# Kernel optimization log

Measured on AMD Instinct MI355X. Metric: run time of the kernel, lower is better.

The kernel has to match this reference:

```python
import jax, jax.numpy as jnp
import numpy as np

# Conv config matching init_kwargs
C_IN, C_OUT = 128, 256
KH, KW = 3, 3
STRIDE = (1, 1)
PADDING = ((1, 1), (1, 1))
DILATION = (1, 1)
B, H, W = 32, 56, 56


def setup_inputs() -> dict:
    key = jax.random.key(0)
    k1, k2, k3 = jax.random.split(key, 3)
    x = jax.random.normal(k1, (B, C_IN, H, W), dtype=jnp.float32)
    # Flattened weight as stored by Conv2DUF: conv.weight.view(O,-1).t() -> [C*kh*kw, O]
    weight = jax.random.normal(k2, (C_IN * KH * KW, C_OUT), dtype=jnp.float32) * 0.02
    bias = jax.random.normal(k3, (C_OUT,), dtype=jnp.float32) * 0.02
    return {"x": x, "weight": weight, "bias": bias}


def reference(x, weight, bias):
    # Conv2DUF computes unfold(x) @ weight + bias, which is exactly a 2D
    # cross-correlation with the original conv kernel. Recover the [O,C,kh,kw]
    # kernel from the flattened [C*kh*kw, O] matrix and use the fused conv
    # primitive (same math, no giant im2col buffer).
    kernel = weight.T.reshape(C_OUT, C_IN, KH, KW)
    out = jax.lax.conv_general_dilated(
        x, kernel,
        window_strides=STRIDE,
        padding=PADDING,
        rhs_dilation=DILATION,
        dimension_numbers=("NCHW", "OIHW", "NCHW"),
    )
    return out + bias[None, :, None, None]
```

## Files before the change

kernel.cpp:

```cpp
#include <hip/hip_runtime.h>
#include <stdint.h>


#define C_INQ 128
#define C_OUTQ 256
#define HDIM 56
#define WDIM 56
#define BDIM 32
#define HP 58
#define WP 58
#define HWPIX (HDIM * WDIM)
#define GSTRIDE (BDIM * HP * WP * 8)
#define XT_ELEMS ((size_t)16 * GSTRIDE)
#define XT_BYTES (XT_ELEMS * 2)

typedef __bf16 bf16x8 __attribute__((ext_vector_type(8)));
typedef unsigned short ushort8 __attribute__((ext_vector_type(8)));
typedef float floatx4 __attribute__((ext_vector_type(4)));

__device__ __forceinline__ unsigned short f2bf(float f) {
  union { float f; unsigned int u; } v; v.f = f;
  unsigned int u = v.u;
  unsigned int r = u + 0x7FFFu + ((u >> 16) & 1u);
  return (unsigned short)(r >> 16);
}
__device__ __forceinline__ unsigned int pack2(float a, float b) {
  return (unsigned int)f2bf(a) | ((unsigned int)f2bf(b) << 16);
}

__global__ __launch_bounds__(256) void pad_transpose_kernel(
    const float* __restrict__ x, unsigned short* __restrict__ xt) {
  const int blk = blockIdx.x;
  const int b = blk / HP;
  const int hp = blk - b * HP;
  const int t = threadIdx.x;
  uint4* __restrict__ xt4 = (uint4*)xt;
  if (hp == 0 || hp == HP - 1) {
    for (int i = t; i < 16 * WP; i += 256) {
      int g = i / WP, wp = i - g * WP;
      xt4[((size_t)(g * BDIM + b) * HP + hp) * WP + wp] = make_uint4(0, 0, 0, 0);
    }
    return;
  }
  const int h = hp - 1;
  if (t < 224) {
    const int g = t / 14;
    const int w4 = (t - g * 14) * 4;
    const float* xp = x + ((size_t)b * C_INQ + g * 8) * HWPIX + h * WDIM + w4;
    float4 L0 = *(const float4*)(xp);
    float4 L1 = *(const float4*)(xp + HWPIX);
    float4 L2 = *(const float4*)(xp + 2 * HWPIX);
    float4 L3 = *(const float4*)(xp + 3 * HWPIX);
    float4 L4 = *(const float4*)(xp + 4 * HWPIX);
    float4 L5 = *(const float4*)(xp + 5 * HWPIX);
    float4 L6 = *(const float4*)(xp + 6 * HWPIX);
    float4 L7 = *(const float4*)(xp + 7 * HWPIX);
    uint4* dst = xt4 + ((size_t)(g * BDIM + b) * HP + hp) * WP + 1 + w4;
    dst[0] = make_uint4(pack2(L0.x, L1.x), pack2(L2.x, L3.x),
                        pack2(L4.x, L5.x), pack2(L6.x, L7.x));
    dst[1] = make_uint4(pack2(L0.y, L1.y), pack2(L2.y, L3.y),
                        pack2(L4.y, L5.y), pack2(L6.y, L7.y));
    dst[2] = make_uint4(pack2(L0.z, L1.z), pack2(L2.z, L3.z),
                        pack2(L4.z, L5.z), pack2(L6.z, L7.z));
    dst[3] = make_uint4(pack2(L0.w, L1.w), pack2(L2.w, L3.w),
                        pack2(L4.w, L5.w), pack2(L6.w, L7.w));
  } else {
    const int r = t - 224;
    const int g = r >> 1;
    const int wp = (r & 1) * (WP - 1);
    xt4[((size_t)(g * BDIM + b) * HP + hp) * WP + wp] = make_uint4(0, 0, 0, 0);
  }
}

__global__ __launch_bounds__(256) void weight_transform_kernel(
    const float* __restrict__ w, unsigned short* __restrict__ wt) {
  const int bx = blockIdx.x;
  const int khw = bx >> 4;
  const int r4 = bx & 15;
  const int n0w = (r4 >> 2) * 64;
  const int c32 = (r4 & 3) * 32;
  const int t = threadIdx.x;
  __shared__ float lds[32 * 66];
#pragma unroll
  for (int r = 0; r < 8; ++r) {
    int idx = r * 256 + t;
    int n = idx & 63, c = idx >> 6;
    lds[c * 66 + n] = w[(size_t)((c32 + c) * 9 + khw) * C_OUTQ + n0w + n];
  }
  __syncthreads();
  {
    int n = t >> 2, c8 = (t & 3) * 8;
    const float* s = lds + c8 * 66 + n;
    uint4 o;
    o.x = pack2(s[0],   s[66]);
    o.y = pack2(s[132], s[198]);
    o.z = pack2(s[264], s[330]);
    o.w = pack2(s[396], s[462]);
    *(uint4*)(wt + (size_t)khw * (C_OUTQ * C_INQ) + (size_t)(n0w + n) * C_INQ + c32 + c8) = o;
  }
}

#define BM 128
#define BN 256
#define BK 32
#define STEPS 36

__global__ __launch_bounds__(256, 2) void conv_gemm_kernel(
    const unsigned short* __restrict__ xt,
    const unsigned short* __restrict__ wt,
    const float* __restrict__ bias,
    float* __restrict__ out) {
  __shared__ __align__(16) unsigned short ldsA[3 * BM * BK];
  __shared__ __align__(16) unsigned short ldsB[3 * BN * BK];

  const int t = threadIdx.x;
  const int lane = t & 63;
  const int wave = t >> 6;
  const int tile_m = blockIdx.x;

  int gbaseA[2], gbaseB[4];
#pragma unroll
  for (int r = 0; r < 2; ++r) {
    int g = r * 256 + t;
    int row = g >> 2;
    int kpart = (g & 3) ^ (row & 3);
    int pix = tile_m * BM + row;
    int b = pix / HWPIX;
    int p = pix - b * HWPIX;
    int h = p / WDIM;
    int w = p - h * WDIM;
    gbaseA[r] = kpart * GSTRIDE + ((b * HP + h) * WP + w) * 8;
  }
#pragma unroll
  for (int r = 0; r < 4; ++r) {
    int g = r * 256 + t;
    int row = g >> 2;
    int kpart = (g & 3) ^ (row & 3);
    gbaseB[r] = row * C_INQ + kpart * 8;
  }

  const int wm = (wave >> 1) * 64;
  const int wn = (wave & 1) * 128;
  const int mrow = lane & 15;
  const int quad = lane >> 4;

  int aoff[4], boff[8];
#pragma unroll
  for (int i = 0; i < 4; ++i) {
    int row = wm + i * 16 + mrow;
    aoff[i] = row * BK + ((quad ^ (row & 3)) * 8);
  }
#pragma unroll
  for (int j = 0; j < 8; ++j) {
    int row = wn + j * 16 + mrow;
    boff[j] = row * BK + ((quad ^ (row & 3)) * 8);
  }

  const int ldst = wave * 64 * 8;

  floatx4 acc[4][8] = {};

  auto stage = [&](int s2, int bufc) {
    const int khw = s2 >> 2;
    const int cq = s2 & 3;
    const int kh = khw / 3;
    const int kw = khw - kh * 3;
    const int koffA = cq * 4 * GSTRIDE + (kh * WP + kw) * 8;
    const int koffB = khw * (C_OUTQ * C_INQ) + cq * 32;
#pragma unroll
    for (int r = 0; r < 2; ++r)
      __builtin_amdgcn_global_load_lds(
          (const __attribute__((address_space(1))) unsigned int*)(xt + gbaseA[r] + koffA),
          (__attribute__((address_space(3))) unsigned int*)(ldsA + bufc * (BM * BK) + r * 2048 + ldst),
          16, 0, 0);
#pragma unroll
    for (int r = 0; r < 4; ++r)
      __builtin_amdgcn_global_load_lds(
          (const __attribute__((address_space(1))) unsigned int*)(wt + gbaseB[r] + koffB),
          (__attribute__((address_space(3))) unsigned int*)(ldsB + bufc * (BN * BK) + r * 2048 + ldst),
          16, 0, 0);
  };

  auto compute_step = [&](int bufc) {
    const unsigned short* A = ldsA + bufc * (BM * BK);
    const unsigned short* B = ldsB + bufc * (BN * BK);
    bf16x8 afr[4], bfr[8];
#pragma unroll
    for (int i = 0; i < 4; ++i)
      afr[i] = __builtin_bit_cast(bf16x8, *(const ushort8*)(A + aoff[i]));
#pragma unroll
    for (int j = 0; j < 8; ++j)
      bfr[j] = __builtin_bit_cast(bf16x8, *(const ushort8*)(B + boff[j]));
#pragma unroll
    for (int i = 0; i < 4; ++i)
#pragma unroll
      for (int j = 0; j < 8; ++j)
        acc[i][j] = __builtin_amdgcn_mfma_f32_16x16x32_bf16(afr[i], bfr[j], acc[i][j], 0, 0, 0);
  };

#define K_STEP(S, BUF, VM, DOSTAGE)                                  \
  {                                                                  \
    asm volatile("s_waitcnt vmcnt(" VM ")" ::: "memory");            \
    __builtin_amdgcn_s_barrier();                                    \
    compute_step(BUF);                                               \
    __builtin_amdgcn_s_barrier();                                    \
    if (DOSTAGE) stage((S) + 3, BUF);                                \
  }

  stage(0, 0);
  stage(1, 1);
  stage(2, 2);

#pragma unroll 1
  for (int so = 0; so < 11; ++so) {
    const int s = so * 3;
    K_STEP(s, 0, "12", true);
    K_STEP(s + 1, 1, "12", true);
    K_STEP(s + 2, 2, "12", true);
  }
  K_STEP(33, 0, "12", false);
  K_STEP(34, 1, "6", false);
  K_STEP(35, 2, "0", false);
#undef K_STEP

  float bv[8];
#pragma unroll
  for (int jn = 0; jn < 8; ++jn) bv[jn] = bias[wn + jn * 16 + mrow];
#pragma unroll
  for (int i = 0; i < 4; ++i) {
    const int mbase = tile_m * BM + wm + i * 16 + quad * 4;
    const int b = mbase / HWPIX;
    const int p = mbase - b * HWPIX;
    float* obase = out + (size_t)b * (C_OUTQ * HWPIX) + p;
#pragma unroll
    for (int jn = 0; jn < 8; ++jn) {
      const int ng = wn + jn * 16 + mrow;
      floatx4 v = acc[i][jn];
      v[0] += bv[jn]; v[1] += bv[jn]; v[2] += bv[jn]; v[3] += bv[jn];
      *(floatx4*)(obase + (size_t)ng * HWPIX) = v;
    }
  }
}

extern "C" void kernel_launch(void* const* d_in, const int* in_sizes, int n_in,
                              void* d_out, int out_size, void* d_ws, size_t ws_size,
                              hipStream_t stream) {
  const float* x    = (const float*)d_in[0];
  const float* w    = (const float*)d_in[1];
  const float* bias = (const float*)d_in[2];
  float* out = (float*)d_out;

  unsigned short* xt = (unsigned short*)d_ws;
  unsigned short* wt = (unsigned short*)((char*)d_ws + XT_BYTES);

  hipLaunchKernelGGL(pad_transpose_kernel, dim3(BDIM * HP), dim3(256), 0, stream, x, xt);
  hipLaunchKernelGGL(weight_transform_kernel, dim3(144), dim3(256), 0, stream, w, wt);
  hipLaunchKernelGGL(conv_gemm_kernel, dim3(784), dim3(256), 0, stream, xt, wt, bias, out);
}
```

Baseline: 234.4 us.

## Merge prep kernels, double-buffer LDS, new swizzle, remap tiles, raise MFMA priority

Folds the input pad/transpose and weight transform into one launch to save a kernel launch. The GEMM moves from triple to double LDS buffering, which cuts LDS use from 72KB to 48KB per block. It also changes the bank swizzle to XOR with (row>>1)&3, remaps block IDs so that consecutive blocks are spread across tiles, and wraps the MFMA loop in s_setprio. The shallower pipeline risks exposing more global-load latency.

```diff
diff --git a/kernel.cpp b/kernel.cpp
--- a/kernel.cpp
+++ b/kernel.cpp
@@ -28,115 +28,117 @@
   return (unsigned int)f2bf(a) | ((unsigned int)f2bf(b) << 16);
 }
 
-__global__ __launch_bounds__(256) void pad_transpose_kernel(
-    const float* __restrict__ x, unsigned short* __restrict__ xt) {
-  const int blk = blockIdx.x;
-  const int b = blk / HP;
-  const int hp = blk - b * HP;
+#define PAD_BLOCKS (BDIM * HP)
+__global__ __launch_bounds__(256) void prep_kernel(
+    const float* __restrict__ x, unsigned short* __restrict__ xt,
+    const float* __restrict__ w, unsigned short* __restrict__ wt) {
   const int t = threadIdx.x;
-  uint4* __restrict__ xt4 = (uint4*)xt;
-  if (hp == 0 || hp == HP - 1) {
-    for (int i = t; i < 16 * WP; i += 256) {
-      int g = i / WP, wp = i - g * WP;
+  if (blockIdx.x < PAD_BLOCKS) {
+    const int blk = blockIdx.x;
+    const int b = blk / HP;
+    const int hp = blk - b * HP;
+    uint4* __restrict__ xt4 = (uint4*)xt;
+    if (hp == 0 || hp == HP - 1) {
+      for (int i = t; i < 16 * WP; i += 256) {
+        int g = i / WP, wp = i - g * WP;
+        xt4[((size_t)(g * BDIM + b) * HP + hp) * WP + wp] = make_uint4(0, 0, 0, 0);
+      }
+      return;
+    }
+    const int h = hp - 1;
+    if (t < 224) {
+      const int g = t / 14;
+      const int w4 = (t - g * 14) * 4;
+      const float* xp = x + ((size_t)b * C_INQ + g * 8) * HWPIX + h * WDIM + w4;
+      float4 L0 = *(const float4*)(xp);
+      float4 L1 = *(const float4*)(xp + HWPIX);
+      float4 L2 = *(const float4*)(xp + 2 * HWPIX);
+      float4 L3 = *(const float4*)(xp + 3 * HWPIX);
+      float4 L4 = *(const float4*)(xp + 4 * HWPIX);
+      float4 L5 = *(const float4*)(xp + 5 * HWPIX);
+      float4 L6 = *(const float4*)(xp + 6 * HWPIX);
+      float4 L7 = *(const float4*)(xp + 7 * HWPIX);
+      uint4* dst = xt4 + ((size_t)(g * BDIM + b) * HP + hp) * WP + 1 + w4;
+      dst[0] = make_uint4(pack2(L0.x, L1.x), pack2(L2.x, L3.x),
+                          pack2(L4.x, L5.x), pack2(L6.x, L7.x));
+      dst[1] = make_uint4(pack2(L0.y, L1.y), pack2(L2.y, L3.y),
+                          pack2(L4.y, L5.y), pack2(L6.y, L7.y));
+      dst[2] = make_uint4(pack2(L0.z, L1.z), pack2(L2.z, L3.z),
+                          pack2(L4.z, L5.z), pack2(L6.z, L7.z));
+      dst[3] = make_uint4(pack2(L0.w, L1.w), pack2(L2.w, L3.w),
+                          pack2(L4.w, L5.w), pack2(L6.w, L7.w));
+    } else {
+      const int r = t - 224;
+      const int g = r >> 1;
+      const int wp = (r & 1) * (WP - 1);
       xt4[((size_t)(g * BDIM + b) * HP + hp) * WP + wp] = make_uint4(0, 0, 0, 0);
     }
-    return;
-  }
-  const int h = hp - 1;
-  if (t < 224) {
-    const int g = t / 14;
-    const int w4 = (t - g * 14) * 4;
-    const float* xp = x + ((size_t)b * C_INQ + g * 8) * HWPIX + h * WDIM + w4;
-    float4 L0 = *(const float4*)(xp);
-    float4 L1 = *(const float4*)(xp + HWPIX);
-    float4 L2 = *(const float4*)(xp + 2 * HWPIX);
-    float4 L3 = *(const float4*)(xp + 3 * HWPIX);
-    float4 L4 = *(const float4*)(xp + 4 * HWPIX);
-    float4 L5 = *(const float4*)(xp + 5 * HWPIX);
-    float4 L6 = *(const float4*)(xp + 6 * HWPIX);
-    float4 L7 = *(const float4*)(xp + 7 * HWPIX);
-    uint4* dst = xt4 + ((size_t)(g * BDIM + b) * HP + hp) * WP + 1 + w4;
-    dst[0] = make_uint4(pack2(L0.x, L1.x), pack2(L2.x, L3.x),
-                        pack2(L4.x, L5.x), pack2(L6.x, L7.x));
-    dst[1] = make_uint4(pack2(L0.y, L1.y), pack2(L2.y, L3.y),
-                        pack2(L4.y, L5.y), pack2(L6.y, L7.y));
-    dst[2] = make_uint4(pack2(L0.z, L1.z), pack2(L2.z, L3.z),
-                        pack2(L4.z, L5.z), pack2(L6.z, L7.z));
-    dst[3] = make_uint4(pack2(L0.w, L1.w), pack2(L2.w, L3.w),
-                        pack2(L4.w, L5.w), pack2(L6.w, L7.w));
   } else {
-    const int r = t - 224;
-    const int g = r >> 1;
-    const int wp = (r & 1) * (WP - 1);
-    xt4[((size_t)(g * BDIM + b) * HP + hp) * WP + wp] = make_uint4(0, 0, 0, 0);
-  }
-}
-
-__global__ __launch_bounds__(256) void weight_transform_kernel(
-    const float* __restrict__ w, unsigned short* __restrict__ wt) {
-  const int bx = blockIdx.x;
-  const int khw = bx >> 4;
-  const int r4 = bx & 15;
-  const int n0w = (r4 >> 2) * 64;
-  const int c32 = (r4 & 3) * 32;
-  const int t = threadIdx.x;
-  __shared__ float lds[32 * 66];
-#pragma unroll
-  for (int r = 0; r < 8; ++r) {
-    int idx = r * 256 + t;
-    int n = idx & 63, c = idx >> 6;
-    lds[c * 66 + n] = w[(size_t)((c32 + c) * 9 + khw) * C_OUTQ + n0w + n];
-  }
-  __syncthreads();
-  {
-    int n = t >> 2, c8 = (t & 3) * 8;
-    const float* s = lds + c8 * 66 + n;
-    uint4 o;
-    o.x = pack2(s[0],   s[66]);
-    o.y = pack2(s[132], s[198]);
-    o.z = pack2(s[264], s[330]);
-    o.w = pack2(s[396], s[462]);
-    *(uint4*)(wt + (size_t)khw * (C_OUTQ * C_INQ) + (size_t)(n0w + n) * C_INQ + c32 + c8) = o;
+    const int bx = blockIdx.x - PAD_BLOCKS;
+    const int khw = bx >> 4;
+    const int r4 = bx & 15;
+    const int n0w = (r4 >> 2) * 64;
+    const int c32 = (r4 & 3) * 32;
+    __shared__ float lds[32 * 66];
+#pragma unroll
+    for (int r = 0; r < 8; ++r) {
+      int idx = r * 256 + t;
+      int n = idx & 63, c = idx >> 6;
+      lds[c * 66 + n] = w[(size_t)((c32 + c) * 9 + khw) * C_OUTQ + n0w + n];
+    }
+    __syncthreads();
+    {
+      int n = t >> 2, c8 = (t & 3) * 8;
+      const float* s = lds + c8 * 66 + n;
+      uint4 o;
+      o.x = pack2(s[0],   s[66]);
+      o.y = pack2(s[132], s[198]);
+      o.z = pack2(s[264], s[330]);
+      o.w = pack2(s[396], s[462]);
+      *(uint4*)(wt + (size_t)khw * (C_OUTQ * C_INQ) + (size_t)(n0w + n) * C_INQ + c32 + c8) = o;
+    }
   }
 }
 
 #define BM 128
 #define BN 256
 #define BK 32
-#define STEPS 36
+#define NSTEP 36
+#define ABUF 4096
+#define BBUF 8192
 
 __global__ __launch_bounds__(256, 2) void conv_gemm_kernel(
     const unsigned short* __restrict__ xt,
     const unsigned short* __restrict__ wt,
     const float* __restrict__ bias,
     float* __restrict__ out) {
-  __shared__ __align__(16) unsigned short ldsA[3 * BM * BK];
-  __shared__ __align__(16) unsigned short ldsB[3 * BN * BK];
+  __shared__ __align__(16) unsigned short ldsA[2 * ABUF];
+  __shared__ __align__(16) unsigned short ldsB[2 * BBUF];
 
   const int t = threadIdx.x;
   const int lane = t & 63;
   const int wave = t >> 6;
-  const int tile_m = blockIdx.x;
+  const int tile_m = ((int)blockIdx.x & 7) * 98 + ((int)blockIdx.x >> 3);
 
   int gbaseA[2], gbaseB[4];
 #pragma unroll
   for (int r = 0; r < 2; ++r) {
     int g = r * 256 + t;
     int row = g >> 2;
-    int kpart = (g & 3) ^ (row & 3);
+    int kg = (g & 3) ^ ((row >> 1) & 3);
     int pix = tile_m * BM + row;
     int b = pix / HWPIX;
     int p = pix - b * HWPIX;
     int h = p / WDIM;
     int w = p - h * WDIM;
-    gbaseA[r] = kpart * GSTRIDE + ((b * HP + h) * WP + w) * 8;
+    gbaseA[r] = kg * GSTRIDE + ((b * HP + h) * WP + w) * 8;
   }
 #pragma unroll
   for (int r = 0; r < 4; ++r) {
     int g = r * 256 + t;
     int row = g >> 2;
-    int kpart = (g & 3) ^ (row & 3);
-    gbaseB[r] = row * C_INQ + kpart * 8;
+    int kg = (g & 3) ^ ((row >> 1) & 3);
+    gbaseB[r] = row * C_INQ + kg * 8;
   }
 
   const int wm = (wave >> 1) * 64;
@@ -147,81 +149,76 @@
   int aoff[4], boff[8];
 #pragma unroll
   for (int i = 0; i < 4; ++i) {
-    int row = wm + i * 16 + mrow;
-    aoff[i] = row * BK + ((quad ^ (row & 3)) * 8);
+    int r = wm + i * 16 + mrow;
+    aoff[i] = r * BK + ((quad ^ ((r >> 1) & 3)) * 8);
   }
 #pragma unroll
   for (int j = 0; j < 8; ++j) {
-    int row = wn + j * 16 + mrow;
-    boff[j] = row * BK + ((quad ^ (row & 3)) * 8);
-  }
-
-  const int ldst = wave * 64 * 8;
+    int n = wn + j * 16 + mrow;
+    boff[j] = n * BK + ((quad ^ ((n >> 1) & 3)) * 8);
+  }
 
   floatx4 acc[4][8] = {};
 
-  auto stage = [&](int s2, int bufc) {
-    const int khw = s2 >> 2;
-    const int cq = s2 & 3;
-    const int kh = khw / 3;
-    const int kw = khw - kh * 3;
+  auto stage = [&](int kt, int buf) {
+    const int khw = kt >> 2, cq = kt & 3;
+    const int kh = khw / 3, kw = khw - kh * 3;
     const int koffA = cq * 4 * GSTRIDE + (kh * WP + kw) * 8;
     const int koffB = khw * (C_OUTQ * C_INQ) + cq * 32;
 #pragma unroll
     for (int r = 0; r < 2; ++r)
       __builtin_amdgcn_global_load_lds(
           (const __attribute__((address_space(1))) unsigned int*)(xt + gbaseA[r] + koffA),
-          (__attribute__((address_space(3))) unsigned int*)(ldsA + bufc * (BM * BK) + r * 2048 + ldst),
+          (__attribute__((address_space(3))) unsigned int*)(ldsA + buf * ABUF + (r * 256 + t) * 8),
           16, 0, 0);
 #pragma unroll
     for (int r = 0; r < 4; ++r)
       __builtin_amdgcn_global_load_lds(
           (const __attribute__((address_space(1))) unsigned int*)(wt + gbaseB[r] + koffB),
-          (__attribute__((address_space(3))) unsigned int*)(ldsB + bufc * (BN * BK) + r * 2048 + ldst),
+          (__attribute__((address_space(3))) unsigned int*)(ldsB + buf * BBUF + (r * 256 + t) * 8),
           16, 0, 0);
   };
 
-  auto compute_step = [&](int bufc) {
-    const unsigned short* A = ldsA + bufc * (BM * BK);
-    const unsigned short* B = ldsB + bufc * (BN * BK);
+#define BC8(p) __builtin_bit_cast(bf16x8, *(const ushort8*)(p))
+
+  auto compute = [&](int buf) {
+    const unsigned short* A = ldsA + buf * ABUF;
+    const unsigned short* B = ldsB + buf * BBUF;
     bf16x8 afr[4], bfr[8];
 #pragma unroll
-    for (int i = 0; i < 4; ++i)
-      afr[i] = __builtin_bit_cast(bf16x8, *(const ushort8*)(A + aoff[i]));
-#pragma unroll
-    for (int j = 0; j < 8; ++j)
-      bfr[j] = __builtin_bit_cast(bf16x8, *(const ushort8*)(B + boff[j]));
+    for (int i = 0; i < 4; ++i) afr[i] = BC8(A + aoff[i]);
+#pragma unroll
+    for (int j = 0; j < 8; ++j) bfr[j] = BC8(B + boff[j]);
+    __builtin_amdgcn_s_setprio(1);
 #pragma unroll
     for (int i = 0; i < 4; ++i)
 #pragma unroll
       for (int j = 0; j < 8; ++j)
         acc[i][j] = __builtin_amdgcn_mfma_f32_16x16x32_bf16(afr[i], bfr[j], acc[i][j], 0, 0, 0);
+    __builtin_amdgcn_s_setprio(0);
   };
 
-#define K_STEP(S, BUF, VM, DOSTAGE)                                  \
+#define K_STEP(KT, BUF, VM, DOSTAGE)                                 \
   {                                                                  \
     asm volatile("s_waitcnt vmcnt(" VM ")" ::: "memory");            \
     __builtin_amdgcn_s_barrier();                                    \
-    compute_step(BUF);                                               \
+    compute(BUF);                                                    \
     __builtin_amdgcn_s_barrier();                                    \
-    if (DOSTAGE) stage((S) + 3, BUF);                                \
+    if (DOSTAGE) stage((KT) + 2, BUF);                               \
   }
 
   stage(0, 0);
   stage(1, 1);
-  stage(2, 2);
 
 #pragma unroll 1
-  for (int so = 0; so < 11; ++so) {
-    const int s = so * 3;
-    K_STEP(s, 0, "12", true);
-    K_STEP(s + 1, 1, "12", true);
-    K_STEP(s + 2, 2, "12", true);
-  }
-  K_STEP(33, 0, "12", false);
-  K_STEP(34, 1, "6", false);
-  K_STEP(35, 2, "0", false);
+  for (int so = 0; so < 17; ++so) {
+    K_STEP(so * 2, 0, "6", true);
+    K_STEP(so * 2 + 1, 1, "6", true);
+  }
+  K_STEP(34, 0, "6", false);
+  K_STEP(35, 1, "0", false);
 #undef K_STEP
+#undef BC8
 
   float bv[8];
 #pragma unroll
@@ -253,7 +250,8 @@
   unsigned short* xt = (unsigned short*)d_ws;
   unsigned short* wt = (unsigned short*)((char*)d_ws + XT_BYTES);
 
-  hipLaunchKernelGGL(pad_transpose_kernel, dim3(BDIM * HP), dim3(256), 0, stream, x, xt);
-  hipLaunchKernelGGL(weight_transform_kernel, dim3(144), dim3(256), 0, stream, w, wt);
-  hipLaunchKernelGGL(conv_gemm_kernel, dim3(784), dim3(256), 0, stream, xt, wt, bias, out);
-}
+  hipLaunchKernelGGL(prep_kernel, dim3(PAD_BLOCKS + 144), dim3(256), 0, stream,
+                     x, xt, w, wt);
+  hipLaunchKernelGGL(conv_gemm_kernel, dim3(784), dim3(256), 0, stream,
+                     xt, wt, bias, out);
+}
```

New measurement: 228.4 us. 2.6% less time.
